# Kernel tuning notes

Measured on AMD Instinct MI355X. Metric: run time of the kernel, lower is better.

## Reference

```python
import jax, jax.numpy as jnp
import numpy as np

N, D, E, H, O, K = 4096, 1024, 8, 4096, 1024, 2
LOSS_COEF = 0.01


def setup_inputs() -> dict:
    key = jax.random.key(0)
    ks = jax.random.split(key, 4)
    scale = lambda k, shape, fan: (jax.random.normal(k, shape, jnp.float32) / np.sqrt(fan).astype(np.float32))
    return {
        "x": jax.random.normal(ks[0], (N, D), jnp.float32),
        "Wg": scale(ks[1], (D, E), D),            # gating network
        "W1": scale(ks[2], (E, D, H), D),          # stacked expert layer 1
        "b1": jnp.zeros((E, H), jnp.float32),
        "W2": scale(ks[3], (E, H, O), H),          # stacked expert layer 2
        "b2": jnp.zeros((E, O), jnp.float32),
        "k": K,
    }


def _cv_squared(v):
    # coefficient-of-variation squared, the tensor2tensor load-balancing loss
    eps = jnp.asarray(1e-10, v.dtype)
    m = jnp.mean(v)
    return jnp.var(v) / (m * m + eps)


def reference(x, Wg, W1, b1, W2, b2, k):
    n, e = x.shape[0], Wg.shape[1]
    # --- top-k gating (deterministic / inference path) ---
    logits = x @ Wg                               # [N, E]
    top_vals, top_idx = jax.lax.top_k(logits, k)  # [N, k]
    top_gates = jax.nn.softmax(top_vals, axis=-1)
    gates = jnp.zeros((n, e), x.dtype).at[jnp.arange(n)[:, None], top_idx].set(top_gates)  # [N, E], sparse rows
    # --- expert compute (dense grouped form of dispatch->expert->combine) ---
    h = jax.nn.relu(jnp.einsum('nd,edh->enh', x, W1) + b1[:, None, :])  # [E, N, H]
    y = jnp.einsum('enh,eho->eno', h, W2) + b2[:, None, :]               # [E, N, O]
    out = jnp.einsum('ne,eno->no', gates, y)                              # weighted combine [N, O]
    # --- auxiliary load-balancing loss ---
    importance = gates.sum(axis=0)                # [E]
    aux_loss = LOSS_COEF * _cv_squared(importance)
    return out, aux_loss
```

## Files before the change

### kernel.cpp

```cpp
#include <hip/hip_runtime.h>
#include <hip/hip_bf16.h>
#include <stdint.h>

#define N_TOK 4096
#define DIM   1024
#define NE    8
#define HID   4096
#define OUTD  1024
#define TOPK  2
#define SLOTS (N_TOK*TOPK)
#define MAXT0 640
#define MAXT1 320

typedef __bf16 bf16_t;
typedef __attribute__((ext_vector_type(8))) __bf16 bf16x8;
typedef __attribute__((ext_vector_type(4))) __bf16 bf16x4;
typedef __attribute__((ext_vector_type(4))) float  f32x4;

static __device__ __forceinline__ uint32_t pk2(float a, float b) {
    __bf16 x = (__bf16)a, y = (__bf16)b;
    return (uint32_t)__builtin_bit_cast(uint16_t, x) |
          ((uint32_t)__builtin_bit_cast(uint16_t, y) << 16);
}

__global__ __launch_bounds__(512)
void k_gating(const float* __restrict__ x, const float* __restrict__ wg,
              bf16_t* __restrict__ xb,
              int* __restrict__ tki, float* __restrict__ tkg) {
    int n = blockIdx.x * 8 + (threadIdx.x >> 6);
    int lane = threadIdx.x & 63;
    const float* xr = x + (size_t)n * DIM;
    double acc[NE];
#pragma unroll
    for (int e = 0; e < NE; ++e) acc[e] = 0.0;
#pragma unroll
    for (int i = 0; i < 4; ++i) {
        int d0 = i * 256 + lane * 4;
        float4 v = *(const float4*)&xr[d0];
        bf16x4 o;
        o[0] = (__bf16)v.x; o[1] = (__bf16)v.y; o[2] = (__bf16)v.z; o[3] = (__bf16)v.w;
        *(bf16x4*)&xb[(size_t)n * DIM + d0] = o;
        const float* wr = wg + (size_t)d0 * NE;
#pragma unroll
        for (int j = 0; j < 4; ++j) {
            double xv = (double)((&v.x)[j]);
#pragma unroll
            for (int e = 0; e < NE; ++e) acc[e] += xv * (double)wr[j * NE + e];
        }
    }
#pragma unroll
    for (int e = 0; e < NE; ++e)
        for (int off = 32; off > 0; off >>= 1) acc[e] += __shfl_xor(acc[e], off);
    if (lane == 0) {
        int i0 = 0; double v0 = acc[0];
#pragma unroll
        for (int e = 1; e < NE; ++e) if (acc[e] > v0) { v0 = acc[e]; i0 = e; }
        int i1 = -1; double v1 = -1e300;
#pragma unroll
        for (int e = 0; e < NE; ++e) if (e != i0 && acc[e] > v1) { v1 = acc[e]; i1 = e; }
        double e1 = exp(v1 - v0);
        double s = 1.0 + e1;
        tki[n*2]   = i0;  tki[n*2+1] = i1;
        tkg[n*2]   = (float)(1.0 / s);
        tkg[n*2+1] = (float)(e1 / s);
    }
}

__global__ __launch_bounds__(256)
void k_route(const int* __restrict__ tki, const float* __restrict__ tkg,
             int* __restrict__ counts, int* __restrict__ bases,
             int* __restrict__ tb0, int* __restrict__ tb1,
             float* __restrict__ aux_out,
             int* __restrict__ tok_ids, int* __restrict__ slotmap) {
    const int e = blockIdx.x, t = threadIdx.x;
    const int wid = t >> 6, lane = t & 63;
    int   lc[NE]; float lg[NE];
#pragma unroll
    for (int k = 0; k < NE; ++k) { lc[k] = 0; lg[k] = 0.f; }
    for (int i = t; i < SLOTS; i += 256) {
        int ee = tki[i]; float gg = tkg[i];
#pragma unroll
        for (int k = 0; k < NE; ++k) if (ee == k) { lc[k]++; lg[k] += gg; }
    }
#pragma unroll
    for (int k = 0; k < NE; ++k)
        for (int off = 32; off > 0; off >>= 1) {
            lc[k] += __shfl_xor(lc[k], off);
            lg[k] += __shfl_xor(lg[k], off);
        }
    __shared__ int   wcI[4][NE];
    __shared__ float wcF[4][NE];
    if (lane == 0)
#pragma unroll
        for (int k = 0; k < NE; ++k) { wcI[wid][k] = lc[k]; wcF[wid][k] = lg[k]; }
    __syncthreads();
    int cnt[NE];
#pragma unroll
    for (int k = 0; k < NE; ++k)
        cnt[k] = wcI[0][k] + wcI[1][k] + wcI[2][k] + wcI[3][k];
    if (e == 0 && t == 0) {
        float gs[NE];
#pragma unroll
        for (int k = 0; k < NE; ++k)
            gs[k] = wcF[0][k] + wcF[1][k] + wcF[2][k] + wcF[3][k];
        float m = 0.f;
        for (int k = 0; k < NE; ++k) m += gs[k];
        m /= (float)NE;
        float var = 0.f;
        for (int k = 0; k < NE; ++k) { float d = gs[k] - m; var += d * d; }
        var /= (float)NE;
        aux_out[0] = 0.01f * var / (m * m + 1e-10f);
        int b = 0, c0 = 0, c1 = 0;
        tb0[0] = 0; tb1[0] = 0;
        for (int k = 0; k < NE; ++k) {
            counts[k] = cnt[k]; bases[k] = b; b += cnt[k];
            int nty = (cnt[k] + 255) >> 8;
            c0 += 16 * nty; c1 += 8 * nty;
            tb0[k+1] = c0; tb1[k+1] = c1;
        }
    }
    int run = 0;
    for (int k = 0; k < e; ++k) run += cnt[k];
    __shared__ int wc[4];
    for (int base = 0; base < SLOTS; base += 256) {
        int i = base + t;
        bool f = (tki[i] == e);
        unsigned long long bl = __ballot(f);
        int pre = __popcll(bl & ((1ull << lane) - 1ull));
        if (lane == 0) wc[wid] = __popcll(bl);
        __syncthreads();
        int woff = 0;
#pragma unroll
        for (int u = 0; u < 4; ++u) if (u < wid) woff += wc[u];
        int tot = wc[0] + wc[1] + wc[2] + wc[3];
        if (f) { int s = run + woff + pre; tok_ids[s] = i >> 1; slotmap[i] = s; }
        run += tot;
        __syncthreads();
    }
}

__global__ __launch_bounds__(512)
void k_transpose(const float* __restrict__ w1, const float* __restrict__ w2,
                 bf16_t* __restrict__ w1t, bf16_t* __restrict__ w2t) {
    __shared__ bf16_t tT[64][264];
    const int bx = blockIdx.x;
    const float* src; bf16_t* dst; int R, C, ry, cx;
    if (bx < 2048) {
        int e = bx >> 8, rem = bx & 255;
        ry = rem >> 6; cx = rem & 63;
        src = w1 + (size_t)e * DIM * HID; dst = w1t + (size_t)e * DIM * HID;
        R = DIM; C = HID;
    } else {
        int b2 = bx - 2048;
        int e = b2 >> 8, rem = b2 & 255;
        ry = rem >> 4; cx = rem & 15;
        src = w2 + (size_t)e * HID * OUTD; dst = w2t + (size_t)e * HID * OUTD;
        R = HID; C = OUTD;
    }
    const int r0 = ry * 256, c0 = cx * 64;
    const int tx = threadIdx.x & 15;
    const int ta = threadIdx.x >> 4;
#pragma unroll
    for (int p = 0; p < 4; ++p) {
        int r = 2 * ta + 64 * p;
        float4 va = *(const float4*)&src[(size_t)(r0 + r)     * C + c0 + tx * 4];
        float4 vb = *(const float4*)&src[(size_t)(r0 + r + 1) * C + c0 + tx * 4];
#pragma unroll
        for (int j = 0; j < 4; ++j)
            *(uint32_t*)&tT[tx * 4 + j][r] = pk2((&va.x)[j], (&vb.x)[j]);
    }
    __syncthreads();
    const int w = threadIdx.x >> 6, l = threadIdx.x & 63;
    const int ccb = w * 2 + (l >> 5);
    const int rb  = (l & 31) * 8;
#pragma unroll
    for (int q = 0; q < 4; ++q) {
        int cc = q * 16 + ccb;
        bf16x8 o = *(const bf16x8*)&tT[cc][rb];
        *(bf16x8*)&dst[(size_t)(c0 + cc) * R + r0 + rb] = o;
    }
}

template <int MODE>
__global__ __launch_bounds__(512, 2)
void k_gemm(const bf16_t* __restrict__ A,
            const bf16_t* __restrict__ Bt,
            const float* __restrict__ bias,
            const int* __restrict__ tok_ids,
            const int* __restrict__ bases,
            const int* __restrict__ counts,
            const int* __restrict__ tb,
            bf16_t* __restrict__ Y) {
    constexpr int KD   = (MODE == 0) ? DIM : HID;
    constexpr int ND   = (MODE == 0) ? HID : OUTD;
    constexpr int KLEN = (MODE == 0) ? DIM : (HID / 2);
    constexpr int KT   = KLEN / 32;
    constexpr int BUFE = 16384;

    const int ti = blockIdx.x;
    if (ti >= tb[NE]) return;
    int e = 0;
#pragma unroll
    for (int k = 1; k < NE; ++k) if (ti >= tb[k]) e = k;
    const int local = ti - tb[e];
    const int ne = counts[e];
    const int b0 = bases[e];
    int panel, y, kslot = 0;
    if (MODE == 0) { y = local >> 4; panel = local & 15; }
    else           { y = local >> 3; int q = local & 7; panel = q >> 1; kslot = q & 1; }
    const int m0 = y * 256, n0 = panel * 256;
    const int koff = (MODE == 0) ? 0 : kslot * KLEN;
    bf16_t* __restrict__ Yw = (MODE == 0) ? Y : (Y + (size_t)kslot * SLOTS * OUTD);

    extern __shared__ bf16_t lds[];

    const int t = threadIdx.x, w = t >> 6, L = t & 63;
    const int wm = w >> 2, wn = w & 3;
    const int lr = L & 15, lq = L >> 4;
    const int srow  = L >> 2;
    const int sslot = L & 3;

    int offA[8], offB[4];
#pragma unroll
    for (int i = 0; i < 8; ++i) {
        int r = wm * 128 + i * 16 + lr;
        offA[i] = r * 32 + ((lq ^ ((r >> 1) & 3)) << 3);
    }
#pragma unroll
    for (int j = 0; j < 4; ++j) {
        int r = wn * 64 + j * 16 + lr;
        offB[j] = 8192 + r * 32 + ((lq ^ ((r >> 1) & 3)) << 3);
    }
    int sdstA[2], sdstB[2];
#pragma unroll
    for (int g = 0; g < 2; ++g) {
        sdstA[g] = (g * 128 + w * 16) * 32;
        sdstB[g] = 8192 + (g * 128 + w * 16) * 32;
    }

#define GLL(srcp, dste) __builtin_amdgcn_global_load_lds( \
        (const __attribute__((address_space(1))) uint32_t*)(srcp), \
        (__attribute__((address_space(3))) uint32_t*)(lds + (dste)), 16, 0, 0)
#define STAGE(Tt, bsl) { \
        _Pragma("unroll") for (int g_ = 0; g_ < 2; ++g_) { \
            GLL(aptr[g_] + (Tt) * 32, (bsl) * BUFE + sdstA[g_]); \
            GLL(bptr[g_] + (Tt) * 32, (bsl) * BUFE + sdstB[g_]); } }

    const bf16_t* aptr[2];
    const bf16_t* bptr[2];
#pragma unroll
    for (int g = 0; g < 2; ++g) {
        int row = g * 128 + w * 16 + srow;
        int gk  = sslot ^ ((row >> 1) & 3);
        int mm = m0 + row;
        int rr = (mm < ne) ? mm : (ne - 1);
        size_t arow = (MODE == 0) ? (size_t)tok_ids[b0 + rr] * KD : (size_t)(b0 + rr) * KD;
        aptr[g] = A + arow + koff + gk * 8;
        bptr[g] = Bt + ((size_t)e * ND + n0 + row) * KD + koff + gk * 8;
    }

    f32x4 acc[8][4];
#pragma unroll
    for (int i = 0; i < 8; ++i)
#pragma unroll
        for (int j = 0; j < 4; ++j) acc[i][j] = (f32x4){0.f, 0.f, 0.f, 0.f};

    STAGE(0, 0); STAGE(1, 1);

    int cb = 0;
    int nb = 2;
    for (int T = 0; T < KT; ++T) {
        if (T < KT - 1) { asm volatile("s_waitcnt vmcnt(4)" ::: "memory"); }
        else            { asm volatile("s_waitcnt vmcnt(0)" ::: "memory"); }
        __builtin_amdgcn_s_barrier();
        if (T + 2 < KT) STAGE(T + 2, nb);

        bf16x8 fb[4], fa[8];
#pragma unroll
        for (int j = 0; j < 4; ++j) fb[j] = *(const bf16x8*)(lds + cb * BUFE + offB[j]);
#pragma unroll
        for (int i = 0; i < 4; ++i) fa[i] = *(const bf16x8*)(lds + cb * BUFE + offA[i]);
        __builtin_amdgcn_sched_barrier(0);
#pragma unroll
        for (int i = 4; i < 8; ++i) fa[i] = *(const bf16x8*)(lds + cb * BUFE + offA[i]);
        __builtin_amdgcn_sched_barrier(0);
        asm volatile("s_waitcnt lgkmcnt(4)" ::: "memory");
        __builtin_amdgcn_sched_barrier(0);
        __builtin_amdgcn_s_setprio(1);
#pragma unroll
        for (int i = 0; i < 4; ++i)
#pragma unroll
            for (int j = 0; j < 4; ++j)
                acc[i][j] = __builtin_amdgcn_mfma_f32_16x16x32_bf16(fb[j], fa[i], acc[i][j], 0, 0, 0);
        __builtin_amdgcn_s_setprio(0);
        asm volatile("s_waitcnt lgkmcnt(0)" ::: "memory");
        __builtin_amdgcn_sched_barrier(0);
        __builtin_amdgcn_s_setprio(1);
#pragma unroll
        for (int i = 4; i < 8; ++i)
#pragma unroll
            for (int j = 0; j < 4; ++j)
                acc[i][j] = __builtin_amdgcn_mfma_f32_16x16x32_bf16(fb[j], fa[i], acc[i][j], 0, 0, 0);
        __builtin_amdgcn_s_setprio(0);

        cb = (cb == 2) ? 0 : cb + 1;
        nb = (nb == 2) ? 0 : nb + 1;
    }

    const int kbias = (MODE == 0) ? 1 : (kslot == 0 ? 1 : 0);
#pragma unroll
    for (int i = 0; i < 8; ++i) {
        int gm = m0 + wm * 128 + i * 16 + lr;
        if (gm < ne) {
#pragma unroll
            for (int j = 0; j < 4; ++j) {
                int gn = n0 + wn * 64 + j * 16 + lq * 4;
                f32x4 bv = *(const f32x4*)&bias[(size_t)e * ND + gn];
                bf16x4 hv;
#pragma unroll
                for (int r = 0; r < 4; ++r) {
                    float v = acc[i][j][r];
                    if (kbias) v += bv[r];
                    if (MODE == 0) v = fmaxf(v, 0.f);
                    hv[r] = (__bf16)v;
                }
                *(bf16x4*)&Yw[(size_t)(b0 + gm) * ND + gn] = hv;
            }
        }
    }
#undef STAGE
#undef GLL
}

__global__ void k_combine(const bf16_t* __restrict__ ybuf,
                          const int* __restrict__ slotmap,
                          const float* __restrict__ tkg,
                          float* __restrict__ out) {
    int n = blockIdx.x;
    int d = threadIdx.x * 4;
    int s0 = slotmap[2 * n], s1 = slotmap[2 * n + 1];
    float g0 = tkg[2 * n],  g1 = tkg[2 * n + 1];
    const bf16_t* y2 = ybuf + (size_t)SLOTS * OUTD;
    bf16x4 a0 = *(const bf16x4*)&ybuf[(size_t)s0 * OUTD + d];
    bf16x4 a1 = *(const bf16x4*)&y2  [(size_t)s0 * OUTD + d];
    bf16x4 c0 = *(const bf16x4*)&ybuf[(size_t)s1 * OUTD + d];
    bf16x4 c1 = *(const bf16x4*)&y2  [(size_t)s1 * OUTD + d];
    f32x4 o;
#pragma unroll
    for (int r = 0; r < 4; ++r)
        o[r] = g0 * ((float)a0[r] + (float)a1[r]) + g1 * ((float)c0[r] + (float)c1[r]);
    *(f32x4*)&out[(size_t)n * OUTD + d] = o;
}

extern "C" void kernel_launch(void* const* d_in, const int* in_sizes, int n_in,
                              void* d_out, int out_size, void* d_ws, size_t ws_size,
                              hipStream_t stream) {
    const float* x  = (const float*)d_in[0];
    const float* wg = (const float*)d_in[1];
    const float* w1 = (const float*)d_in[2];
    const float* b1 = (const float*)d_in[3];
    const float* w2 = (const float*)d_in[4];
    const float* b2 = (const float*)d_in[5];
    float* out = (float*)d_out;

    char* ws = (char*)d_ws;
    size_t o = 0;
    auto alloc = [&](size_t b) { size_t r = o; o = (o + b + 255) & ~(size_t)255; return r; };
    int*    counts  = (int*)(ws + alloc(NE * 4));
    int*    bases   = (int*)(ws + alloc(NE * 4));
    int*    tb0     = (int*)(ws + alloc((NE + 1) * 4));
    int*    tb1     = (int*)(ws + alloc((NE + 1) * 4));
    int*    tki     = (int*)(ws + alloc(SLOTS * 4));
    float*  tkg     = (float*)(ws + alloc(SLOTS * 4));
    int*    tok_ids = (int*)(ws + alloc(SLOTS * 4));
    int*    slotmap = (int*)(ws + alloc(SLOTS * 4));
    bf16_t* xb      = (bf16_t*)(ws + alloc((size_t)N_TOK * DIM * 2));
    size_t  w1t_off = alloc((size_t)NE * HID * DIM * 2);
    bf16_t* w1t     = (bf16_t*)(ws + w1t_off);
    bf16_t* ybuf    = (bf16_t*)(ws + w1t_off);
    bf16_t* w2t     = (bf16_t*)(ws + alloc((size_t)NE * OUTD * HID * 2));
    bf16_t* hbuf    = (bf16_t*)(ws + alloc((size_t)SLOTS * HID * 2));
    (void)ws_size; (void)n_in; (void)in_sizes;

    hipFuncSetAttribute((const void*)&k_gemm<0>, hipFuncAttributeMaxDynamicSharedMemorySize, 98304);
    hipFuncSetAttribute((const void*)&k_gemm<1>, hipFuncAttributeMaxDynamicSharedMemorySize, 98304);

    k_gating<<<N_TOK / 8, 512, 0, stream>>>(x, wg, xb, tki, tkg);
    k_route<<<NE, 256, 0, stream>>>(tki, tkg, counts, bases, tb0, tb1,
                                    out + (size_t)N_TOK * OUTD, tok_ids, slotmap);
    k_transpose<<<4096, 512, 0, stream>>>(w1, w2, w1t, w2t);

    k_gemm<0><<<MAXT0, 512, 98304, stream>>>(xb, w1t, b1, tok_ids, bases, counts, tb0, hbuf);
    k_gemm<1><<<MAXT1, 512, 98304, stream>>>(hbuf, w2t, b2, tok_ids, bases, counts, tb1, ybuf);

    k_combine<<<N_TOK, 256, 0, stream>>>(ybuf, slotmap, tkg, out);
}
```

Baseline: 340.7 us.

## Persistent per-XCD work-queue grouped GEMM with 128-row tiles and 4-way split-K

The fixed-grid grouped GEMM becomes a persistent kernel. Workgroups pull tile indices from a per-XCD atomic cursor over a tile table that the routing kernel builds, with one contiguous range of the table per XCD. Tiles shrink from 256x256 to 128x256, which cuts the padding waste on ragged expert row counts and lowers LDS use so occupancy can rise. The second GEMM splits K four ways instead of two, and the combine kernel sums four partial buffers. The cost is lower arithmetic intensity per tile, twice the partial-output traffic for the second GEMM, atomic and barrier overhead per tile, and an extra memset launch.

```diff
diff --git a/kernel.cpp b/kernel.cpp
--- a/kernel.cpp
+++ b/kernel.cpp
@@ -9,8 +9,7 @@
 #define OUTD  1024
 #define TOPK  2
 #define SLOTS (N_TOK*TOPK)
-#define MAXT0 640
-#define MAXT1 320
+#define MAXTAB 1280
 
 typedef __bf16 bf16_t;
 typedef __attribute__((ext_vector_type(8))) __bf16 bf16x8;
@@ -69,7 +68,8 @@
 __global__ __launch_bounds__(256)
 void k_route(const int* __restrict__ tki, const float* __restrict__ tkg,
              int* __restrict__ counts, int* __restrict__ bases,
-             int* __restrict__ tb0, int* __restrict__ tb1,
+             int* __restrict__ tab0, int* __restrict__ tab1,
+             int* __restrict__ xs0, int* __restrict__ xs1,
              float* __restrict__ aux_out,
              int* __restrict__ tok_ids, int* __restrict__ slotmap) {
     const int e = blockIdx.x, t = threadIdx.x;
@@ -110,13 +110,22 @@
         for (int k = 0; k < NE; ++k) { float d = gs[k] - m; var += d * d; }
         var /= (float)NE;
         aux_out[0] = 0.01f * var / (m * m + 1e-10f);
-        int b = 0, c0 = 0, c1 = 0;
-        tb0[0] = 0; tb1[0] = 0;
+        int b = 0;
+        for (int k = 0; k < NE; ++k) { counts[k] = cnt[k]; bases[k] = b; b += cnt[k]; }
+        int tot0 = 0, tot1 = 0;
         for (int k = 0; k < NE; ++k) {
-            counts[k] = cnt[k]; bases[k] = b; b += cnt[k];
-            int nty = (cnt[k] + 255) >> 8;
-            c0 += 16 * nty; c1 += 8 * nty;
-            tb0[k+1] = c0; tb1[k+1] = c1;
+            int nty = (cnt[k] + 127) >> 7;
+            for (int p = 0; p < 16; ++p)
+                for (int y = 0; y < nty; ++y)
+                    tab0[tot0++] = (k << 16) | (p << 8) | y;
+            for (int ks = 0; ks < 4; ++ks)
+                for (int p = 0; p < 4; ++p)
+                    for (int y = 0; y < nty; ++y)
+                        tab1[tot1++] = (k << 16) | (ks << 12) | (p << 8) | y;
+        }
+        for (int xq = 0; xq <= 8; ++xq) {
+            xs0[xq] = (int)(((long long)tot0 * xq) / 8);
+            xs1[xq] = (int)(((long long)tot1 * xq) / 8);
         }
     }
     int run = 0;
@@ -182,35 +191,25 @@
 }
 
 template <int MODE>
-__global__ __launch_bounds__(512, 2)
+__global__ __launch_bounds__(512, 4)
 void k_gemm(const bf16_t* __restrict__ A,
             const bf16_t* __restrict__ Bt,
             const float* __restrict__ bias,
             const int* __restrict__ tok_ids,
             const int* __restrict__ bases,
             const int* __restrict__ counts,
-            const int* __restrict__ tb,
+            const int* __restrict__ tab,
+            const int* __restrict__ xs,
+            int* __restrict__ cursor,
             bf16_t* __restrict__ Y) {
     constexpr int KD   = (MODE == 0) ? DIM : HID;
     constexpr int ND   = (MODE == 0) ? HID : OUTD;
-    constexpr int KLEN = (MODE == 0) ? DIM : (HID / 2);
+    constexpr int KLEN = 1024;
     constexpr int KT   = KLEN / 32;
-    constexpr int BUFE = 16384;
-
-    const int ti = blockIdx.x;
-    if (ti >= tb[NE]) return;
-    int e = 0;
-#pragma unroll
-    for (int k = 1; k < NE; ++k) if (ti >= tb[k]) e = k;
-    const int local = ti - tb[e];
-    const int ne = counts[e];
-    const int b0 = bases[e];
-    int panel, y, kslot = 0;
-    if (MODE == 0) { y = local >> 4; panel = local & 15; }
-    else           { y = local >> 3; int q = local & 7; panel = q >> 1; kslot = q & 1; }
-    const int m0 = y * 256, n0 = panel * 256;
-    const int koff = (MODE == 0) ? 0 : kslot * KLEN;
-    bf16_t* __restrict__ Yw = (MODE == 0) ? Y : (Y + (size_t)kslot * SLOTS * OUTD);
+    constexpr int BUFE = 12288;
+
+    const int xcd = blockIdx.x & 7;
+    const int beg = xs[xcd], end = xs[xcd + 1];
 
     extern __shared__ bf16_t lds[];
 
@@ -220,111 +219,110 @@
     const int srow  = L >> 2;
     const int sslot = L & 3;
 
-    int offA[8], offB[4];
-#pragma unroll
-    for (int i = 0; i < 8; ++i) {
-        int r = wm * 128 + i * 16 + lr;
+    int offA[4], offB[4];
+#pragma unroll
+    for (int i = 0; i < 4; ++i) {
+        int r = wm * 64 + i * 16 + lr;
         offA[i] = r * 32 + ((lq ^ ((r >> 1) & 3)) << 3);
     }
 #pragma unroll
     for (int j = 0; j < 4; ++j) {
         int r = wn * 64 + j * 16 + lr;
-        offB[j] = 8192 + r * 32 + ((lq ^ ((r >> 1) & 3)) << 3);
-    }
-    int sdstA[2], sdstB[2];
-#pragma unroll
-    for (int g = 0; g < 2; ++g) {
-        sdstA[g] = (g * 128 + w * 16) * 32;
-        sdstB[g] = 8192 + (g * 128 + w * 16) * 32;
-    }
+        offB[j] = 4096 + r * 32 + ((lq ^ ((r >> 1) & 3)) << 3);
+    }
+    const int sdstA  = (w * 16) * 32;
+    const int sdstB0 = 4096 + (w * 32) * 32;
+    const int sdstB1 = 4096 + (w * 32 + 16) * 32;
 
 #define GLL(srcp, dste) __builtin_amdgcn_global_load_lds( \
         (const __attribute__((address_space(1))) uint32_t*)(srcp), \
         (__attribute__((address_space(3))) uint32_t*)(lds + (dste)), 16, 0, 0)
 #define STAGE(Tt, bsl) { \
-        _Pragma("unroll") for (int g_ = 0; g_ < 2; ++g_) { \
-            GLL(aptr[g_] + (Tt) * 32, (bsl) * BUFE + sdstA[g_]); \
-            GLL(bptr[g_] + (Tt) * 32, (bsl) * BUFE + sdstB[g_]); } }
-
-    const bf16_t* aptr[2];
-    const bf16_t* bptr[2];
-#pragma unroll
-    for (int g = 0; g < 2; ++g) {
-        int row = g * 128 + w * 16 + srow;
-        int gk  = sslot ^ ((row >> 1) & 3);
-        int mm = m0 + row;
-        int rr = (mm < ne) ? mm : (ne - 1);
-        size_t arow = (MODE == 0) ? (size_t)tok_ids[b0 + rr] * KD : (size_t)(b0 + rr) * KD;
-        aptr[g] = A + arow + koff + gk * 8;
-        bptr[g] = Bt + ((size_t)e * ND + n0 + row) * KD + koff + gk * 8;
-    }
-
-    f32x4 acc[8][4];
-#pragma unroll
-    for (int i = 0; i < 8; ++i)
-#pragma unroll
-        for (int j = 0; j < 4; ++j) acc[i][j] = (f32x4){0.f, 0.f, 0.f, 0.f};
-
-    STAGE(0, 0); STAGE(1, 1);
-
-    int cb = 0;
-    int nb = 2;
-    for (int T = 0; T < KT; ++T) {
-        if (T < KT - 1) { asm volatile("s_waitcnt vmcnt(4)" ::: "memory"); }
-        else            { asm volatile("s_waitcnt vmcnt(0)" ::: "memory"); }
-        __builtin_amdgcn_s_barrier();
-        if (T + 2 < KT) STAGE(T + 2, nb);
-
-        bf16x8 fb[4], fa[8];
-#pragma unroll
-        for (int j = 0; j < 4; ++j) fb[j] = *(const bf16x8*)(lds + cb * BUFE + offB[j]);
-#pragma unroll
-        for (int i = 0; i < 4; ++i) fa[i] = *(const bf16x8*)(lds + cb * BUFE + offA[i]);
-        __builtin_amdgcn_sched_barrier(0);
-#pragma unroll
-        for (int i = 4; i < 8; ++i) fa[i] = *(const bf16x8*)(lds + cb * BUFE + offA[i]);
-        __builtin_amdgcn_sched_barrier(0);
-        asm volatile("s_waitcnt lgkmcnt(4)" ::: "memory");
-        __builtin_amdgcn_sched_barrier(0);
-        __builtin_amdgcn_s_setprio(1);
+        GLL(aptr  + (Tt) * 32, (bsl) * BUFE + sdstA); \
+        GLL(bptr0 + (Tt) * 32, (bsl) * BUFE + sdstB0); \
+        GLL(bptr1 + (Tt) * 32, (bsl) * BUFE + sdstB1); }
+
+    __shared__ int sh_ti;
+    for (;;) {
+        if (t == 0) sh_ti = beg + atomicAdd(&cursor[xcd], 1);
+        __syncthreads();
+        const int ti = sh_ti;
+        if (ti >= end) break;
+
+        const int ent   = tab[ti];
+        const int e     = ent >> 16;
+        const int kslot = (ent >> 12) & 15;
+        const int panel = (ent >> 8) & 15;
+        const int y     = ent & 255;
+        const int ne = counts[e];
+        const int b0 = bases[e];
+        const int m0 = y * 128, n0 = panel * 256;
+        const int koff = kslot * KLEN;
+        bf16_t* __restrict__ Yw = (MODE == 0) ? Y : (Y + (size_t)kslot * SLOTS * OUTD);
+
+        int arow_i = m0 + w * 16 + srow;
+        int arr = (arow_i < ne) ? arow_i : (ne - 1);
+        int gka = sslot ^ ((arow_i >> 1) & 3);
+        size_t arow = (MODE == 0) ? (size_t)tok_ids[b0 + arr] * KD : (size_t)(b0 + arr) * KD;
+        const bf16_t* aptr = A + arow + koff + gka * 8;
+        int brow0 = w * 32 + srow;
+        int brow1 = w * 32 + 16 + srow;
+        const bf16_t* bptr0 = Bt + ((size_t)e * ND + n0 + brow0) * KD + koff + ((sslot ^ ((brow0 >> 1) & 3)) * 8);
+        const bf16_t* bptr1 = Bt + ((size_t)e * ND + n0 + brow1) * KD + koff + ((sslot ^ ((brow1 >> 1) & 3)) * 8);
+
+        f32x4 acc[4][4];
 #pragma unroll
         for (int i = 0; i < 4; ++i)
 #pragma unroll
-            for (int j = 0; j < 4; ++j)
-                acc[i][j] = __builtin_amdgcn_mfma_f32_16x16x32_bf16(fb[j], fa[i], acc[i][j], 0, 0, 0);
-        __builtin_amdgcn_s_setprio(0);
-        asm volatile("s_waitcnt lgkmcnt(0)" ::: "memory");
-        __builtin_amdgcn_sched_barrier(0);
-        __builtin_amdgcn_s_setprio(1);
-#pragma unroll
-        for (int i = 4; i < 8; ++i)
-#pragma unroll
-            for (int j = 0; j < 4; ++j)
-                acc[i][j] = __builtin_amdgcn_mfma_f32_16x16x32_bf16(fb[j], fa[i], acc[i][j], 0, 0, 0);
-        __builtin_amdgcn_s_setprio(0);
-
-        cb = (cb == 2) ? 0 : cb + 1;
-        nb = (nb == 2) ? 0 : nb + 1;
-    }
-
-    const int kbias = (MODE == 0) ? 1 : (kslot == 0 ? 1 : 0);
-#pragma unroll
-    for (int i = 0; i < 8; ++i) {
-        int gm = m0 + wm * 128 + i * 16 + lr;
-        if (gm < ne) {
-#pragma unroll
-            for (int j = 0; j < 4; ++j) {
-                int gn = n0 + wn * 64 + j * 16 + lq * 4;
-                f32x4 bv = *(const f32x4*)&bias[(size_t)e * ND + gn];
-                bf16x4 hv;
-#pragma unroll
-                for (int r = 0; r < 4; ++r) {
-                    float v = acc[i][j][r];
-                    if (kbias) v += bv[r];
-                    if (MODE == 0) v = fmaxf(v, 0.f);
-                    hv[r] = (__bf16)v;
+            for (int j = 0; j < 4; ++j) acc[i][j] = (f32x4){0.f, 0.f, 0.f, 0.f};
+
+        STAGE(0, 0); STAGE(1, 1);
+
+        int cb = 0, nb = 2;
+        for (int T = 0; T < KT; ++T) {
+            if (T < KT - 1) { asm volatile("s_waitcnt vmcnt(3)" ::: "memory"); }
+            else            { asm volatile("s_waitcnt vmcnt(0)" ::: "memory"); }
+            __builtin_amdgcn_s_barrier();
+            if (T + 2 < KT) STAGE(T + 2, nb);
+
+            bf16x8 fa[4], fb[4];
+#pragma unroll
+            for (int j = 0; j < 4; ++j) fb[j] = *(const bf16x8*)(lds + cb * BUFE + offB[j]);
+#pragma unroll
+            for (int i = 0; i < 4; ++i) fa[i] = *(const bf16x8*)(lds + cb * BUFE + offA[i]);
+            asm volatile("s_waitcnt lgkmcnt(0)" ::: "memory");
+            __builtin_amdgcn_sched_barrier(0);
+            __builtin_amdgcn_s_setprio(1);
+#pragma unroll
+            for (int i = 0; i < 4; ++i)
+#pragma unroll
+                for (int j = 0; j < 4; ++j)
+                    acc[i][j] = __builtin_amdgcn_mfma_f32_16x16x32_bf16(fb[j], fa[i], acc[i][j], 0, 0, 0);
+            __builtin_amdgcn_s_setprio(0);
+
+            cb = (cb == 2) ? 0 : cb + 1;
+            nb = (nb == 2) ? 0 : nb + 1;
+        }
+
+        const int kbias = (MODE == 0) ? 1 : (kslot == 0 ? 1 : 0);
+#pragma unroll
+        for (int i = 0; i < 4; ++i) {
+            int gm = m0 + wm * 64 + i * 16 + lr;
+            if (gm < ne) {
+#pragma unroll
+                for (int j = 0; j < 4; ++j) {
+                    int gn = n0 + wn * 64 + j * 16 + lq * 4;
+                    f32x4 bv = *(const f32x4*)&bias[(size_t)e * ND + gn];
+                    bf16x4 hv;
+#pragma unroll
+                    for (int r = 0; r < 4; ++r) {
+                        float v = acc[i][j][r];
+                        if (kbias) v += bv[r];
+                        if (MODE == 0) v = fmaxf(v, 0.f);
+                        hv[r] = (__bf16)v;
+                    }
+                    *(bf16x4*)&Yw[(size_t)(b0 + gm) * ND + gn] = hv;
                 }
-                *(bf16x4*)&Yw[(size_t)(b0 + gm) * ND + gn] = hv;
             }
         }
     }
@@ -340,15 +338,16 @@
     int d = threadIdx.x * 4;
     int s0 = slotmap[2 * n], s1 = slotmap[2 * n + 1];
     float g0 = tkg[2 * n],  g1 = tkg[2 * n + 1];
-    const bf16_t* y2 = ybuf + (size_t)SLOTS * OUTD;
-    bf16x4 a0 = *(const bf16x4*)&ybuf[(size_t)s0 * OUTD + d];
-    bf16x4 a1 = *(const bf16x4*)&y2  [(size_t)s0 * OUTD + d];
-    bf16x4 c0 = *(const bf16x4*)&ybuf[(size_t)s1 * OUTD + d];
-    bf16x4 c1 = *(const bf16x4*)&y2  [(size_t)s1 * OUTD + d];
-    f32x4 o;
-#pragma unroll
-    for (int r = 0; r < 4; ++r)
-        o[r] = g0 * ((float)a0[r] + (float)a1[r]) + g1 * ((float)c0[r] + (float)c1[r]);
+    f32x4 o = (f32x4){0.f, 0.f, 0.f, 0.f};
+#pragma unroll
+    for (int s = 0; s < 4; ++s) {
+        const bf16_t* ys = ybuf + (size_t)s * SLOTS * OUTD;
+        bf16x4 u = *(const bf16x4*)&ys[(size_t)s0 * OUTD + d];
+        bf16x4 v = *(const bf16x4*)&ys[(size_t)s1 * OUTD + d];
+#pragma unroll
+        for (int r = 0; r < 4; ++r)
+            o[r] += g0 * (float)u[r] + g1 * (float)v[r];
+    }
     *(f32x4*)&out[(size_t)n * OUTD + d] = o;
 }
 
@@ -364,12 +363,16 @@
     float* out = (float*)d_out;
 
     char* ws = (char*)d_ws;
-    size_t o = 0;
+    int* cur0 = (int*)(ws + 0);
+    int* cur1 = (int*)(ws + 64);
+    size_t o = 256;
     auto alloc = [&](size_t b) { size_t r = o; o = (o + b + 255) & ~(size_t)255; return r; };
     int*    counts  = (int*)(ws + alloc(NE * 4));
     int*    bases   = (int*)(ws + alloc(NE * 4));
-    int*    tb0     = (int*)(ws + alloc((NE + 1) * 4));
-    int*    tb1     = (int*)(ws + alloc((NE + 1) * 4));
+    int*    xs0     = (int*)(ws + alloc(9 * 4));
+    int*    xs1     = (int*)(ws + alloc(9 * 4));
+    int*    tab0    = (int*)(ws + alloc(MAXTAB * 4));
+    int*    tab1    = (int*)(ws + alloc(MAXTAB * 4));
     int*    tki     = (int*)(ws + alloc(SLOTS * 4));
     float*  tkg     = (float*)(ws + alloc(SLOTS * 4));
     int*    tok_ids = (int*)(ws + alloc(SLOTS * 4));
@@ -382,16 +385,20 @@
     bf16_t* hbuf    = (bf16_t*)(ws + alloc((size_t)SLOTS * HID * 2));
     (void)ws_size; (void)n_in; (void)in_sizes;
 
-    hipFuncSetAttribute((const void*)&k_gemm<0>, hipFuncAttributeMaxDynamicSharedMemorySize, 98304);
-    hipFuncSetAttribute((const void*)&k_gemm<1>, hipFuncAttributeMaxDynamicSharedMemorySize, 98304);
+    hipFuncSetAttribute((const void*)&k_gemm<0>, hipFuncAttributeMaxDynamicSharedMemorySize, 73728);
+    hipFuncSetAttribute((const void*)&k_gemm<1>, hipFuncAttributeMaxDynamicSharedMemorySize, 73728);
+
+    hipMemsetAsync(ws, 0, 256, stream);
 
     k_gating<<<N_TOK / 8, 512, 0, stream>>>(x, wg, xb, tki, tkg);
-    k_route<<<NE, 256, 0, stream>>>(tki, tkg, counts, bases, tb0, tb1,
+    k_route<<<NE, 256, 0, stream>>>(tki, tkg, counts, bases, tab0, tab1, xs0, xs1,
                                     out + (size_t)N_TOK * OUTD, tok_ids, slotmap);
     k_transpose<<<4096, 512, 0, stream>>>(w1, w2, w1t, w2t);
 
-    k_gemm<0><<<MAXT0, 512, 98304, stream>>>(xb, w1t, b1, tok_ids, bases, counts, tb0, hbuf);
-    k_gemm<1><<<MAXT1, 512, 98304, stream>>>(hbuf, w2t, b2, tok_ids, bases, counts, tb1, ybuf);
+    k_gemm<0><<<512, 512, 73728, stream>>>(xb, w1t, b1, tok_ids, bases, counts,
+                                           tab0, xs0, cur0, hbuf);
+    k_gemm<1><<<512, 512, 73728, stream>>>(hbuf, w2t, b2, tok_ids, bases, counts,
+                                           tab1, xs1, cur1, ybuf);
 
     k_combine<<<N_TOK, 256, 0, stream>>>(ybuf, slotmap, tkg, out);
 }
```

Result: slower. 781.1 us (+129.3%).

## Precompute XCD-aware GEMM tile schedule table in routing kernel

Applied to the files above, without the earlier changes.

The routing kernel now builds explicit per-block tile tables for both expert GEMMs. Tiles are laid out in panel-major order per expert and then interleaved so that each of eight block-ID residues receives a contiguous chunk of tiles. The GEMM kernels decode expert, k-slot, panel and row-tile from the table instead of computing them from prefix offsets. The intent is to keep tiles that share weight panels on the same XCD, improving L2 reuse. The cost is a serial single-thread table build, with large local arrays, inside the route kernel.

```diff
diff --git a/kernel.cpp b/kernel.cpp
--- a/kernel.cpp
+++ b/kernel.cpp
@@ -69,7 +69,7 @@
 __global__ __launch_bounds__(256)
 void k_route(const int* __restrict__ tki, const float* __restrict__ tkg,
              int* __restrict__ counts, int* __restrict__ bases,
-             int* __restrict__ tb0, int* __restrict__ tb1,
+             int* __restrict__ tab0, int* __restrict__ tab1,
              float* __restrict__ aux_out,
              int* __restrict__ tok_ids, int* __restrict__ slotmap) {
     const int e = blockIdx.x, t = threadIdx.x;
@@ -110,13 +110,31 @@
         for (int k = 0; k < NE; ++k) { float d = gs[k] - m; var += d * d; }
         var /= (float)NE;
         aux_out[0] = 0.01f * var / (m * m + 1e-10f);
-        int b = 0, c0 = 0, c1 = 0;
-        tb0[0] = 0; tb1[0] = 0;
+        int b = 0;
+        for (int k = 0; k < NE; ++k) { counts[k] = cnt[k]; bases[k] = b; b += cnt[k]; }
+        int lin0[MAXT0], lin1[MAXT1];
+        int tot0 = 0, tot1 = 0;
         for (int k = 0; k < NE; ++k) {
-            counts[k] = cnt[k]; bases[k] = b; b += cnt[k];
             int nty = (cnt[k] + 255) >> 8;
-            c0 += 16 * nty; c1 += 8 * nty;
-            tb0[k+1] = c0; tb1[k+1] = c1;
+            for (int p = 0; p < 16; ++p)
+                for (int y = 0; y < nty; ++y)
+                    lin0[tot0++] = (k << 16) | (p << 8) | y;
+            for (int ks = 0; ks < 2; ++ks)
+                for (int p = 0; p < 4; ++p)
+                    for (int y = 0; y < nty; ++y)
+                        lin1[tot1++] = (k << 16) | (ks << 12) | (p << 8) | y;
+        }
+        for (int i = 0; i < MAXT0; ++i) tab0[i] = -1;
+        for (int i = 0; i < MAXT1; ++i) tab1[i] = -1;
+        for (int r = 0; r < 8; ++r) {
+            int lo = (int)(((long long)tot0 * r) / 8);
+            int hi = (int)(((long long)tot0 * (r + 1)) / 8);
+            for (int c = 0; c < hi - lo; ++c) tab0[c * 8 + r] = lin0[lo + c];
+        }
+        for (int r = 0; r < 8; ++r) {
+            int lo = (int)(((long long)tot1 * r) / 8);
+            int hi = (int)(((long long)tot1 * (r + 1)) / 8);
+            for (int c = 0; c < hi - lo; ++c) tab1[c * 8 + r] = lin1[lo + c];
         }
     }
     int run = 0;
@@ -189,7 +207,7 @@
             const int* __restrict__ tok_ids,
             const int* __restrict__ bases,
             const int* __restrict__ counts,
-            const int* __restrict__ tb,
+            const int* __restrict__ tab,
             bf16_t* __restrict__ Y) {
     constexpr int KD   = (MODE == 0) ? DIM : HID;
     constexpr int ND   = (MODE == 0) ? HID : OUTD;
@@ -197,17 +215,14 @@
     constexpr int KT   = KLEN / 32;
     constexpr int BUFE = 16384;
 
-    const int ti = blockIdx.x;
-    if (ti >= tb[NE]) return;
-    int e = 0;
-#pragma unroll
-    for (int k = 1; k < NE; ++k) if (ti >= tb[k]) e = k;
-    const int local = ti - tb[e];
+    const int ent = tab[blockIdx.x];
+    if (ent < 0) return;
+    const int e     = ent >> 16;
+    const int kslot = (ent >> 12) & 15;
+    const int panel = (ent >> 8) & 15;
+    const int y     = ent & 255;
     const int ne = counts[e];
     const int b0 = bases[e];
-    int panel, y, kslot = 0;
-    if (MODE == 0) { y = local >> 4; panel = local & 15; }
-    else           { y = local >> 3; int q = local & 7; panel = q >> 1; kslot = q & 1; }
     const int m0 = y * 256, n0 = panel * 256;
     const int koff = (MODE == 0) ? 0 : kslot * KLEN;
     bf16_t* __restrict__ Yw = (MODE == 0) ? Y : (Y + (size_t)kslot * SLOTS * OUTD);
@@ -368,8 +383,8 @@
     auto alloc = [&](size_t b) { size_t r = o; o = (o + b + 255) & ~(size_t)255; return r; };
     int*    counts  = (int*)(ws + alloc(NE * 4));
     int*    bases   = (int*)(ws + alloc(NE * 4));
-    int*    tb0     = (int*)(ws + alloc((NE + 1) * 4));
-    int*    tb1     = (int*)(ws + alloc((NE + 1) * 4));
+    int*    tab0    = (int*)(ws + alloc(MAXT0 * 4));
+    int*    tab1    = (int*)(ws + alloc(MAXT1 * 4));
     int*    tki     = (int*)(ws + alloc(SLOTS * 4));
     float*  tkg     = (float*)(ws + alloc(SLOTS * 4));
     int*    tok_ids = (int*)(ws + alloc(SLOTS * 4));
@@ -386,12 +401,12 @@
     hipFuncSetAttribute((const void*)&k_gemm<1>, hipFuncAttributeMaxDynamicSharedMemorySize, 98304);
 
     k_gating<<<N_TOK / 8, 512, 0, stream>>>(x, wg, xb, tki, tkg);
-    k_route<<<NE, 256, 0, stream>>>(tki, tkg, counts, bases, tb0, tb1,
+    k_route<<<NE, 256, 0, stream>>>(tki, tkg, counts, bases, tab0, tab1,
                                     out + (size_t)N_TOK * OUTD, tok_ids, slotmap);
     k_transpose<<<4096, 512, 0, stream>>>(w1, w2, w1t, w2t);
 
-    k_gemm<0><<<MAXT0, 512, 98304, stream>>>(xb, w1t, b1, tok_ids, bases, counts, tb0, hbuf);
-    k_gemm<1><<<MAXT1, 512, 98304, stream>>>(hbuf, w2t, b2, tok_ids, bases, counts, tb1, ybuf);
+    k_gemm<0><<<MAXT0, 512, 98304, stream>>>(xb, w1t, b1, tok_ids, bases, counts, tab0, hbuf);
+    k_gemm<1><<<MAXT1, 512, 98304, stream>>>(hbuf, w2t, b2, tok_ids, bases, counts, tab1, ybuf);
 
     k_combine<<<N_TOK, 256, 0, stream>>>(ybuf, slotmap, tkg, out);
 }
```

New measurement: 556.9 us. 1.63x slower.
